# Kernel tuning notes

Measured on AMD Instinct MI355X. Metric: run time of the kernel, lower is better.

Reference implementation:

```python
import jax, jax.numpy as jnp
import numpy as np

WS = (7, 7, 7)          # (Wz, Wh, Ww)
NUM_HEADS = 3


def rel_position_index(ws):
    # Faithful to meshgrid_3d in the source: arrays are reversed, grid i varies
    # along axis i, so coords are stacked in (w, h, z) order.
    wz, wh, ww = ws
    g = np.meshgrid(np.arange(ww), np.arange(wh), np.arange(wz), indexing='ij')
    coords = np.stack(g)                      # (3, ww, wh, wz)
    flat = coords.reshape(3, -1)              # (3, N)
    rel = flat[:, :, None] - flat[:, None, :]  # (3, N, N)
    rel = rel.transpose(1, 2, 0).astype(np.int64)  # (N, N, 3)
    rel[:, :, 0] += wz - 1
    rel[:, :, 1] += wh - 1
    rel[:, :, 2] += ww - 1
    rel[:, :, 0] *= (2 * wh - 1) * (2 * ww - 1)
    rel[:, :, 1] *= (2 * ww - 1)
    return rel.sum(-1)                        # (N, N) in [0, (2W-1)^3)


REL_IDX = jnp.asarray(rel_position_index(WS).reshape(-1), dtype=jnp.int32)


def setup_inputs() -> dict:
    key = jax.random.key(0)
    ks = jax.random.split(key, 6)
    B, N, C = 256, 343, 96
    nW = 32
    x = jax.random.normal(ks[0], (B, N, C), dtype=jnp.float32)
    # shifted-window mask: 0 where attendable, -100 where blocked
    keep = jax.random.uniform(ks[1], (nW, N, N)) < 0.9
    mask = jnp.where(keep, 0.0, -100.0).astype(jnp.float32)
    w_qkv = jax.random.normal(ks[2], (C, 3 * C), dtype=jnp.float32) * 0.05
    b_qkv = jnp.zeros((3 * C,), jnp.float32)
    bias_table = jax.random.normal(ks[3], (2197, NUM_HEADS), dtype=jnp.float32) * 0.02
    w_proj = jax.random.normal(ks[4], (C, C), dtype=jnp.float32) * 0.05
    b_proj = jnp.zeros((C,), jnp.float32)
    return {"x": x, "mask": mask, "w_qkv": w_qkv, "b_qkv": b_qkv,
            "bias_table": bias_table, "w_proj": w_proj, "b_proj": b_proj}


def reference(x, mask, w_qkv, b_qkv, bias_table, w_proj, b_proj):
    B, N, C = x.shape
    H = NUM_HEADS
    hd = C // H
    scale = hd ** -0.5  # qk_scale is None -> head_dim**-0.5 (swin v1 path)
    # QKV projection, split to heads: (3, B, H, N, hd)
    qkv = (x @ w_qkv + b_qkv).reshape(B, N, 3, H, hd).transpose(2, 0, 3, 1, 4)
    q, k, v = qkv[0] * scale, qkv[1], qkv[2]
    attn = jnp.einsum('bhnd,bhmd->bhnm', q, k)        # (B, H, N, N)
    # gathered relative-position bias -> (H, N, N)
    bias = bias_table[REL_IDX].reshape(N, N, H).transpose(2, 0, 1)
    attn = attn + bias[None]
    # shifted-window mask add: reshape to (B//nW, nW, H, N, N)
    nW = mask.shape[0]
    attn = attn.reshape(B // nW, nW, H, N, N) + mask[None, :, None]
    attn = jax.nn.softmax(attn.reshape(B, H, N, N), axis=-1)
    out = jnp.einsum('bhnm,bhmd->bhnd', attn, v)      # (B, H, N, hd)
    out = out.transpose(0, 2, 1, 3).reshape(B, N, C)
    return out @ w_proj + b_proj
```

## Files before the change

kernel.cpp:

```cpp
#include <hip/hip_runtime.h>

#define N_TOK 343
#define NP 352
#define C_DIM 96
#define HEADS 3
#define HD 32
#define B_SZ 256
#define NW 32
#define QKV_COLS 288

#define QKV_ELEMS (B_SZ * HEADS * N_TOK * HD)
#define X2_ELEMS ((long)B_SZ * N_TOK * C_DIM)
#define CMB_ELEMS ((long)NW * HEADS * N_TOK * NP)

typedef _Float16 f16;
typedef _Float16 f16x2 __attribute__((ext_vector_type(2)));
typedef _Float16 f16x4 __attribute__((ext_vector_type(4)));
typedef _Float16 f16x8 __attribute__((ext_vector_type(8)));
typedef float f32x4 __attribute__((ext_vector_type(4)));

__global__ __launch_bounds__(256) void wprep_kernel(
    const float* __restrict__ w_qkv, const float* __restrict__ w_proj,
    f16* __restrict__ wt_qkv, f16* __restrict__ wt_proj) {
  const int e = blockIdx.x * 256 + threadIdx.x;
  if (e < QKV_COLS * 96) {
    const int cc = e / 96, k = e % 96;
    wt_qkv[e] = (f16)w_qkv[k * QKV_COLS + cc];
  } else {
    const int e2 = e - QKV_COLS * 96;
    if (e2 < 96 * 96) {
      const int cc = e2 / 96, k = e2 % 96;
      wt_proj[e2] = (f16)w_proj[k * 96 + cc];
    }
  }
}

__global__ __launch_bounds__(256) void cmb_kernel(
    const float* __restrict__ mask, const float* __restrict__ bias_table,
    f16* __restrict__ cmb) {
  const long e = (long)blockIdx.x * 256 + threadIdx.x;
  if (e >= CMB_ELEMS) return;
  const int key = (int)(e % NP);
  const long rowid = e / NP;
  const int q = (int)(rowid % N_TOK);
  const int wh = (int)(rowid / N_TOK);
  const int h = wh % HEADS;
  const int w = wh / HEADS;
  float val;
  if (key < N_TOK) {
    const int bn = (q / 49) * 169 + ((q / 7) % 7) * 13 + (q % 7);
    const int bm = (key / 49) * 169 + ((key / 7) % 7) * 13 + (key % 7);
    val = bias_table[(bn - bm + 1098) * HEADS + h] +
          mask[((long)w * N_TOK + q) * N_TOK + key];
  } else {
    val = -1000.f;
  }
  cmb[e] = (f16)val;
}

__global__ __launch_bounds__(256) void qkv_mfma_kernel(
    const float* __restrict__ x, const f16* __restrict__ wt,
    const float* __restrict__ bias,
    f16* __restrict__ Q, f16* __restrict__ K, f16* __restrict__ V) {
  const int tid = threadIdx.x;
  const int wave = tid >> 6, lane = tid & 63;
  const int c = lane & 15, g = lane >> 4;
  const long rowTile = (long)blockIdx.x * 64 + wave * 16;
  const long arow = rowTile + c;

  f16x8 af[3];
#pragma unroll
  for (int ks = 0; ks < 3; ++ks) {
    const float* px = x + arow * 96 + ks * 32 + g * 8;
    const float4 lo = *(const float4*)px;
    const float4 hi = *(const float4*)(px + 4);
    f16x8 v;
    v[0] = (f16)lo.x; v[1] = (f16)lo.y; v[2] = (f16)lo.z; v[3] = (f16)lo.w;
    v[4] = (f16)hi.x; v[5] = (f16)hi.y; v[6] = (f16)hi.z; v[7] = (f16)hi.w;
    af[ks] = v;
  }

  int bidx[4], nidx[4];
#pragma unroll
  for (int r = 0; r < 4; ++r) {
    const int row = (int)rowTile + 4 * g + r;
    bidx[r] = row / N_TOK;
    nidx[r] = row % N_TOK;
  }

  const f32x4 zero = {0.f, 0.f, 0.f, 0.f};
  const float scale = 0.17677669529663687f;

#pragma unroll
  for (int ct = 0; ct < 18; ++ct) {
    f32x4 acc = zero;
#pragma unroll
    for (int ks = 0; ks < 3; ++ks) {
      const f16x8 bf = *(const f16x8*)(wt + (ct * 16 + c) * 96 + ks * 32 + g * 8);
      acc = __builtin_amdgcn_mfma_f32_16x16x32_f16(af[ks], bf, acc, 0, 0, 0);
    }
    const int col = ct * 16 + c;
    const int which = ct / 6;
    const int h = (ct % 6) >> 1;
    const int d = ((ct & 1) << 4) + c;
    const float bv = bias[col];
    f16* dst = (which == 0) ? Q : (which == 1) ? K : V;
    const float mult = (which == 0) ? scale : 1.0f;
#pragma unroll
    for (int r = 0; r < 4; ++r) {
      const float v = (acc[r] + bv) * mult;
      dst[(((long)bidx[r] * HEADS + h) * N_TOK + nidx[r]) * HD + d] = (f16)v;
    }
  }
}

__global__ __launch_bounds__(512) void attn_kernel(
    const f16* __restrict__ Qh, const f16* __restrict__ Kh,
    const f16* __restrict__ Vh, const f16* __restrict__ CMB,
    f16* __restrict__ X2h) {
  __shared__ f16 Ks[NP][40];
  __shared__ f16 Vt[HD][360];
  __shared__ f16 Pb[8][16][40];

  const int blk = blockIdx.x;
  const int b = blk / HEADS;
  const int h = blk % HEADS;
  const int tid = threadIdx.x;
  const int wave = tid >> 6;
  const int lane = tid & 63;
  const int c = lane & 15;
  const int g = lane >> 4;

  const f16* Kg = Kh + (long)blk * (N_TOK * HD);
  const f16* Vg = Vh + (long)blk * (N_TOK * HD);
  const f16* Qg = Qh + (long)blk * (N_TOK * HD);

  for (int u = tid; u < NP * 4; u += 512) {
    const int key = u >> 2, j = u & 3;
    f16x8 val = {0, 0, 0, 0, 0, 0, 0, 0};
    if (key < N_TOK) val = *(const f16x8*)(Kg + key * HD + j * 8);
    *(f16x8*)&Ks[key][j * 8] = val;
  }
  for (int i = tid; i < N_TOK * 16; i += 512) {
    const int n = i >> 4, dp = i & 15;
    const f16x2 v2 = *(const f16x2*)(Vg + n * HD + dp * 2);
    Vt[2 * dp][n] = v2.x;
    Vt[2 * dp + 1][n] = v2.y;
  }
  for (int i = tid; i < HD * 9; i += 512) Vt[i / 9][N_TOK + i % 9] = (f16)0;
  __syncthreads();

  const int w = b & (NW - 1);
  const f32x4 zero = {0.f, 0.f, 0.f, 0.f};

  for (int qt = wave; qt < NP / 16; qt += 8) {
    const int q = qt * 16 + c;
    const int qrow = (q < N_TOK) ? q : (N_TOK - 1);
    const f16x8 qf = *(const f16x8*)(Qg + qrow * HD + g * 8);
    const f16* cmrow = CMB + ((long)(w * HEADS + h) * N_TOK + qrow) * NP;

    f32x4 acc0 = zero, acc1 = zero;
    float lsum = 0.f;

    for (int kt = 0; kt < NP / 32; ++kt) {
      const f16x8 kf0 = *(const f16x8*)&Ks[32 * kt + c][g * 8];
      const f16x8 kf1 = *(const f16x8*)&Ks[32 * kt + 16 + c][g * 8];
      const f16x4 cm0 = *(const f16x4*)(cmrow + 32 * kt + 4 * g);
      const f16x4 cm1 = *(const f16x4*)(cmrow + 32 * kt + 16 + 4 * g);

      const f32x4 s0 = __builtin_amdgcn_mfma_f32_16x16x32_f16(kf0, qf, zero, 0, 0, 0);
      const f32x4 s1 = __builtin_amdgcn_mfma_f32_16x16x32_f16(kf1, qf, zero, 0, 0, 0);

      float p0[4], p1[4];
#pragma unroll
      for (int r = 0; r < 4; ++r) {
        p0[r] = __expf(s0[r] + (float)cm0[r]);
        p1[r] = __expf(s1[r] + (float)cm1[r]);
        lsum += p0[r] + p1[r];
      }
      const f16x2 l0 = __builtin_bit_cast(f16x2, __builtin_amdgcn_cvt_pkrtz(p0[0], p0[1]));
      const f16x2 h0 = __builtin_bit_cast(f16x2, __builtin_amdgcn_cvt_pkrtz(p0[2], p0[3]));
      const f16x2 l1 = __builtin_bit_cast(f16x2, __builtin_amdgcn_cvt_pkrtz(p1[0], p1[1]));
      const f16x2 h1 = __builtin_bit_cast(f16x2, __builtin_amdgcn_cvt_pkrtz(p1[2], p1[3]));
      f16x4 pk0, pk1;
      pk0.x = l0.x; pk0.y = l0.y; pk0.z = h0.x; pk0.w = h0.y;
      pk1.x = l1.x; pk1.y = l1.y; pk1.z = h1.x; pk1.w = h1.y;
      *(f16x4*)&Pb[wave][c][4 * g] = pk0;
      *(f16x4*)&Pb[wave][c][16 + 4 * g] = pk1;
      __builtin_amdgcn_wave_barrier();

      const f16x8 pf = *(const f16x8*)&Pb[wave][c][8 * g];
      const f16x8 vf0 = *(const f16x8*)&Vt[c][32 * kt + 8 * g];
      const f16x8 vf1 = *(const f16x8*)&Vt[16 + c][32 * kt + 8 * g];
      acc0 = __builtin_amdgcn_mfma_f32_16x16x32_f16(vf0, pf, acc0, 0, 0, 0);
      acc1 = __builtin_amdgcn_mfma_f32_16x16x32_f16(vf1, pf, acc1, 0, 0, 0);
      __builtin_amdgcn_wave_barrier();
    }

    lsum += __shfl_xor(lsum, 16);
    lsum += __shfl_xor(lsum, 32);
    const float inv = 1.f / lsum;

    if (q < N_TOK) {
      f16* orow = X2h + ((long)b * N_TOK + q) * C_DIM + h * HD;
      f16x4 o0, o1;
#pragma unroll
      for (int r = 0; r < 4; ++r) {
        o0[r] = (f16)(acc0[r] * inv);
        o1[r] = (f16)(acc1[r] * inv);
      }
      *(f16x4*)(orow + 4 * g) = o0;
      *(f16x4*)(orow + 16 + 4 * g) = o1;
    }
  }
}

__global__ __launch_bounds__(256) void proj_mfma_kernel(
    const f16* __restrict__ X2h, const f16* __restrict__ wt,
    const float* __restrict__ bias, float* __restrict__ out) {
  const int tid = threadIdx.x;
  const int wave = tid >> 6, lane = tid & 63;
  const int c = lane & 15, g = lane >> 4;
  const long rowTile = (long)blockIdx.x * 64 + wave * 16;
  const long arow = rowTile + c;

  f16x8 af[3];
#pragma unroll
  for (int ks = 0; ks < 3; ++ks)
    af[ks] = *(const f16x8*)(X2h + arow * 96 + ks * 32 + g * 8);

  const f32x4 zero = {0.f, 0.f, 0.f, 0.f};
#pragma unroll
  for (int ct = 0; ct < 6; ++ct) {
    f32x4 acc = zero;
#pragma unroll
    for (int ks = 0; ks < 3; ++ks) {
      const f16x8 bf = *(const f16x8*)(wt + (ct * 16 + c) * 96 + ks * 32 + g * 8);
      acc = __builtin_amdgcn_mfma_f32_16x16x32_f16(af[ks], bf, acc, 0, 0, 0);
    }
    const int col = ct * 16 + c;
    const float bv = bias[col];
#pragma unroll
    for (int r = 0; r < 4; ++r)
      out[(rowTile + 4 * g + r) * 96 + col] = acc[r] + bv;
  }
}

extern "C" void kernel_launch(void* const* d_in, const int* in_sizes, int n_in,
                              void* d_out, int out_size, void* d_ws, size_t ws_size,
                              hipStream_t stream) {
  const float* x          = (const float*)d_in[0];
  const float* mask       = (const float*)d_in[1];
  const float* w_qkv      = (const float*)d_in[2];
  const float* b_qkv      = (const float*)d_in[3];
  const float* bias_table = (const float*)d_in[4];
  const float* w_proj     = (const float*)d_in[5];
  const float* b_proj     = (const float*)d_in[6];
  float* out = (float*)d_out;

  f16* Qh = (f16*)d_ws;
  f16* Kh = Qh + QKV_ELEMS;
  f16* Vh = Kh + QKV_ELEMS;
  f16* X2h = Vh + QKV_ELEMS;
  f16* CMB = X2h + X2_ELEMS;
  f16* WTQ = CMB + CMB_ELEMS;
  f16* WTP = WTQ + QKV_COLS * 96;

  const int cmbBlocks = (int)((CMB_ELEMS + 255) / 256);
  const int wBlocks = (QKV_COLS * 96 + 96 * 96 + 255) / 256;
  const int gemmBlocks = (B_SZ * N_TOK) / 64;

  wprep_kernel<<<wBlocks, 256, 0, stream>>>(w_qkv, w_proj, WTQ, WTP);
  cmb_kernel<<<cmbBlocks, 256, 0, stream>>>(mask, bias_table, CMB);
  qkv_mfma_kernel<<<gemmBlocks, 256, 0, stream>>>(x, WTQ, b_qkv, Qh, Kh, Vh);
  attn_kernel<<<B_SZ * HEADS, 512, 0, stream>>>(Qh, Kh, Vh, CMB, X2h);
  proj_mfma_kernel<<<gemmBlocks, 256, 0, stream>>>(X2h, WTP, b_proj, out);
}
```

Measured before the change: 216.2 us.

## Coalesce QKV/proj stores via LDS staging and drop K and P shared buffers in attention

The QKV kernel now stages Q and K tiles per wave in shared memory so each lane writes a contiguous 16-byte chunk instead of scattered 2-byte stores. The proj kernel likewise stages its output tile in LDS and writes float4 rows. In the attention kernel, K is read straight from global/L2 rather than staged in LDS, and the P fragment is built in registers instead of going through a shared-memory round trip. Together with smaller LDS and a launch-bounds occupancy hint, this aims to cut LDS traffic and raise occupancy, at the cost of extra global K reads per wave.

```diff
diff --git a/kernel.cpp b/kernel.cpp
--- a/kernel.cpp
+++ b/kernel.cpp
@@ -62,6 +62,7 @@
     const float* __restrict__ x, const f16* __restrict__ wt,
     const float* __restrict__ bias,
     f16* __restrict__ Q, f16* __restrict__ K, f16* __restrict__ V) {
+  __shared__ f16 sh[4][16][40];
   const int tid = threadIdx.x;
   const int wave = tid >> 6, lane = tid & 63;
   const int c = lane & 15, g = lane >> 4;
@@ -80,6 +81,8 @@
     af[ks] = v;
   }
 
+  const int rowL = (int)rowTile + (lane >> 2);
+  const int bL = rowL / N_TOK, nL = rowL % N_TOK;
   int bidx[4], nidx[4];
 #pragma unroll
   for (int r = 0; r < 4; ++r) {
@@ -92,35 +95,48 @@
   const float scale = 0.17677669529663687f;
 
 #pragma unroll
-  for (int ct = 0; ct < 18; ++ct) {
-    f32x4 acc = zero;
-#pragma unroll
-    for (int ks = 0; ks < 3; ++ks) {
-      const f16x8 bf = *(const f16x8*)(wt + (ct * 16 + c) * 96 + ks * 32 + g * 8);
-      acc = __builtin_amdgcn_mfma_f32_16x16x32_f16(af[ks], bf, acc, 0, 0, 0);
-    }
-    const int col = ct * 16 + c;
-    const int which = ct / 6;
-    const int h = (ct % 6) >> 1;
-    const int d = ((ct & 1) << 4) + c;
-    const float bv = bias[col];
-    f16* dst = (which == 0) ? Q : (which == 1) ? K : V;
+  for (int p = 0; p < 9; ++p) {
+    const int which = p / 3;
+    const int h = p % 3;
     const float mult = (which == 0) ? scale : 1.0f;
 #pragma unroll
-    for (int r = 0; r < 4; ++r) {
-      const float v = (acc[r] + bv) * mult;
-      dst[(((long)bidx[r] * HEADS + h) * N_TOK + nidx[r]) * HD + d] = (f16)v;
-    }
-  }
-}
-
-__global__ __launch_bounds__(512) void attn_kernel(
+    for (int e = 0; e < 2; ++e) {
+      const int ct = 2 * p + e;
+      f32x4 acc = zero;
+#pragma unroll
+      for (int ks = 0; ks < 3; ++ks) {
+        const f16x8 bf = *(const f16x8*)(wt + (ct * 16 + c) * 96 + ks * 32 + g * 8);
+        acc = __builtin_amdgcn_mfma_f32_16x16x32_f16(af[ks], bf, acc, 0, 0, 0);
+      }
+      const float bv = bias[ct * 16 + c];
+      if (which < 2) {
+#pragma unroll
+        for (int r = 0; r < 4; ++r)
+          sh[wave][4 * g + r][(e << 4) + c] = (f16)((acc[r] + bv) * mult);
+      } else {
+        const int d = ((ct & 1) << 4) + c;
+#pragma unroll
+        for (int r = 0; r < 4; ++r) {
+          V[(((long)bidx[r] * HEADS + h) * N_TOK + nidx[r]) * HD + d] =
+              (f16)(acc[r] + bv);
+        }
+      }
+    }
+    if (which < 2) {
+      __builtin_amdgcn_wave_barrier();
+      const f16x8 po = *(const f16x8*)&sh[wave][lane >> 2][(lane & 3) * 8];
+      __builtin_amdgcn_wave_barrier();
+      f16* dst = (which == 0) ? Q : K;
+      *(f16x8*)(dst + (((long)bL * HEADS + h) * N_TOK + nL) * HD + (lane & 3) * 8) = po;
+    }
+  }
+}
+
+__global__ __launch_bounds__(512, 6) void attn_kernel(
     const f16* __restrict__ Qh, const f16* __restrict__ Kh,
     const f16* __restrict__ Vh, const f16* __restrict__ CMB,
     f16* __restrict__ X2h) {
-  __shared__ f16 Ks[NP][40];
-  __shared__ f16 Vt[HD][360];
-  __shared__ f16 Pb[8][16][40];
+  __shared__ f16 Vt[HD][356];
 
   const int blk = blockIdx.x;
   const int b = blk / HEADS;
@@ -135,19 +151,13 @@
   const f16* Vg = Vh + (long)blk * (N_TOK * HD);
   const f16* Qg = Qh + (long)blk * (N_TOK * HD);
 
-  for (int u = tid; u < NP * 4; u += 512) {
-    const int key = u >> 2, j = u & 3;
-    f16x8 val = {0, 0, 0, 0, 0, 0, 0, 0};
-    if (key < N_TOK) val = *(const f16x8*)(Kg + key * HD + j * 8);
-    *(f16x8*)&Ks[key][j * 8] = val;
-  }
   for (int i = tid; i < N_TOK * 16; i += 512) {
     const int n = i >> 4, dp = i & 15;
     const f16x2 v2 = *(const f16x2*)(Vg + n * HD + dp * 2);
     Vt[2 * dp][n] = v2.x;
     Vt[2 * dp + 1][n] = v2.y;
   }
-  for (int i = tid; i < HD * 9; i += 512) Vt[i / 9][N_TOK + i % 9] = (f16)0;
+  for (int i = tid; i < HD * 13; i += 512) Vt[i / 13][N_TOK + i % 13] = (f16)0;
   __syncthreads();
 
   const int w = b & (NW - 1);
@@ -163,8 +173,8 @@
     float lsum = 0.f;
 
     for (int kt = 0; kt < NP / 32; ++kt) {
-      const f16x8 kf0 = *(const f16x8*)&Ks[32 * kt + c][g * 8];
-      const f16x8 kf1 = *(const f16x8*)&Ks[32 * kt + 16 + c][g * 8];
+      const f16x8 kf0 = *(const f16x8*)(Kg + (32 * kt + c) * HD + g * 8);
+      const f16x8 kf1 = *(const f16x8*)(Kg + (32 * kt + 16 + c) * HD + g * 8);
       const f16x4 cm0 = *(const f16x4*)(cmrow + 32 * kt + 4 * g);
       const f16x4 cm1 = *(const f16x4*)(cmrow + 32 * kt + 16 + 4 * g);
 
@@ -178,23 +188,23 @@
         p1[r] = __expf(s1[r] + (float)cm1[r]);
         lsum += p0[r] + p1[r];
       }
-      const f16x2 l0 = __builtin_bit_cast(f16x2, __builtin_amdgcn_cvt_pkrtz(p0[0], p0[1]));
-      const f16x2 h0 = __builtin_bit_cast(f16x2, __builtin_amdgcn_cvt_pkrtz(p0[2], p0[3]));
-      const f16x2 l1 = __builtin_bit_cast(f16x2, __builtin_amdgcn_cvt_pkrtz(p1[0], p1[1]));
-      const f16x2 h1 = __builtin_bit_cast(f16x2, __builtin_amdgcn_cvt_pkrtz(p1[2], p1[3]));
-      f16x4 pk0, pk1;
-      pk0.x = l0.x; pk0.y = l0.y; pk0.z = h0.x; pk0.w = h0.y;
-      pk1.x = l1.x; pk1.y = l1.y; pk1.z = h1.x; pk1.w = h1.y;
-      *(f16x4*)&Pb[wave][c][4 * g] = pk0;
-      *(f16x4*)&Pb[wave][c][16 + 4 * g] = pk1;
-      __builtin_amdgcn_wave_barrier();
-
-      const f16x8 pf = *(const f16x8*)&Pb[wave][c][8 * g];
-      const f16x8 vf0 = *(const f16x8*)&Vt[c][32 * kt + 8 * g];
-      const f16x8 vf1 = *(const f16x8*)&Vt[16 + c][32 * kt + 8 * g];
+      const f16x2 a0 = __builtin_bit_cast(f16x2, __builtin_amdgcn_cvt_pkrtz(p0[0], p0[1]));
+      const f16x2 a1 = __builtin_bit_cast(f16x2, __builtin_amdgcn_cvt_pkrtz(p0[2], p0[3]));
+      const f16x2 a2 = __builtin_bit_cast(f16x2, __builtin_amdgcn_cvt_pkrtz(p1[0], p1[1]));
+      const f16x2 a3 = __builtin_bit_cast(f16x2, __builtin_amdgcn_cvt_pkrtz(p1[2], p1[3]));
+      const f16x4 plo = __builtin_shufflevector(a0, a1, 0, 1, 2, 3);
+      const f16x4 phi = __builtin_shufflevector(a2, a3, 0, 1, 2, 3);
+      const f16x8 pf = __builtin_shufflevector(plo, phi, 0, 1, 2, 3, 4, 5, 6, 7);
+
+      const f16x4 va0 = *(const f16x4*)&Vt[c][32 * kt + 4 * g];
+      const f16x4 va1 = *(const f16x4*)&Vt[c][32 * kt + 16 + 4 * g];
+      const f16x4 vb0 = *(const f16x4*)&Vt[16 + c][32 * kt + 4 * g];
+      const f16x4 vb1 = *(const f16x4*)&Vt[16 + c][32 * kt + 16 + 4 * g];
+      const f16x8 vf0 = __builtin_shufflevector(va0, va1, 0, 1, 2, 3, 4, 5, 6, 7);
+      const f16x8 vf1 = __builtin_shufflevector(vb0, vb1, 0, 1, 2, 3, 4, 5, 6, 7);
+
       acc0 = __builtin_amdgcn_mfma_f32_16x16x32_f16(vf0, pf, acc0, 0, 0, 0);
       acc1 = __builtin_amdgcn_mfma_f32_16x16x32_f16(vf1, pf, acc1, 0, 0, 0);
-      __builtin_amdgcn_wave_barrier();
     }
 
     lsum += __shfl_xor(lsum, 16);
@@ -218,6 +228,7 @@
 __global__ __launch_bounds__(256) void proj_mfma_kernel(
     const f16* __restrict__ X2h, const f16* __restrict__ wt,
     const float* __restrict__ bias, float* __restrict__ out) {
+  __shared__ float shp[4][16][100];
   const int tid = threadIdx.x;
   const int wave = tid >> 6, lane = tid & 63;
   const int c = lane & 15, g = lane >> 4;
@@ -238,11 +249,18 @@
       const f16x8 bf = *(const f16x8*)(wt + (ct * 16 + c) * 96 + ks * 32 + g * 8);
       acc = __builtin_amdgcn_mfma_f32_16x16x32_f16(af[ks], bf, acc, 0, 0, 0);
     }
-    const int col = ct * 16 + c;
-    const float bv = bias[col];
+    const float bv = bias[ct * 16 + c];
 #pragma unroll
     for (int r = 0; r < 4; ++r)
-      out[(rowTile + 4 * g + r) * 96 + col] = acc[r] + bv;
+      shp[wave][4 * g + r][ct * 16 + c] = acc[r] + bv;
+  }
+  __builtin_amdgcn_wave_barrier();
+#pragma unroll
+  for (int i = 0; i < 6; ++i) {
+    const int u = lane + 64 * i;
+    const int row = u / 24, ch = u % 24;
+    const float4 v = *(const float4*)&shp[wave][row][ch * 4];
+    *(float4*)(out + (rowTile + row) * 96 + ch * 4) = v;
   }
 }
 
```

Result: slower. 384.0 us (+77.7%).
